# Kernel optimization log

Hardware: AMD Instinct MI355X
Metric: run time of the kernel (lower is better)

## Reference

```python
import jax, jax.numpy as jnp
from jax import lax
import numpy as np

S = 2048      # seq_len
E = 1024      # embedding_dim
H = 512       # hidden per direction (hidden_dim // 2)
V = 50000     # vocab
T = 16        # tagset_size
START, STOP = 0, 1
NEG = -10000.0


def setup_inputs() -> dict:
    key = jax.random.key(0)
    ks = jax.random.split(key, 20)
    bound = 1.0 / np.sqrt(H)

    def u(k, shape):
        return jax.random.uniform(k, shape, minval=-bound, maxval=bound, dtype=jnp.float32)

    sentence = jax.random.randint(ks[0], (S,), 0, V)
    emb = jax.random.normal(ks[1], (V, E), dtype=jnp.float32) * 0.1
    # PyTorch LSTM weights, gate order (i, f, g, o) stacked along first dim
    Wih_f = u(ks[2], (4 * H, E)); Whh_f = u(ks[3], (4 * H, H))
    bih_f = u(ks[4], (4 * H,));   bhh_f = u(ks[5], (4 * H,))
    Wih_b = u(ks[6], (4 * H, E)); Whh_b = u(ks[7], (4 * H, H))
    bih_b = u(ks[8], (4 * H,));   bhh_b = u(ks[9], (4 * H,))
    # init_hidden(): randn initial (h0, c0), [2 directions, H] (batch=1 squeezed)
    h0 = jax.random.normal(ks[10], (2, H), dtype=jnp.float32)
    c0 = jax.random.normal(ks[11], (2, H), dtype=jnp.float32)
    Wout = u(ks[12], (T, 2 * H)); bout = u(ks[13], (T,))
    transitions = jax.random.normal(ks[14], (T, T), dtype=jnp.float32)
    transitions = transitions.at[START, :].set(NEG).at[:, STOP].set(NEG)
    return dict(sentence=sentence, emb=emb,
                Wih_f=Wih_f, Whh_f=Whh_f, bih_f=bih_f, bhh_f=bhh_f,
                Wih_b=Wih_b, Whh_b=Whh_b, bih_b=bih_b, bhh_b=bhh_b,
                h0=h0, c0=c0, Wout=Wout, bout=bout, transitions=transitions)


def _lstm_dir(x, Wih, Whh, bih, bhh, h0, c0):
    # x: [S, E] -> hs: [S, H]; PyTorch gate order i, f, g, o
    xg = x @ Wih.T + bih + bhh  # precompute input contribution [S, 4H]

    def step(carry, xg_t):
        h, c = carry
        g = xg_t + h @ Whh.T
        i, f, gg, o = jnp.split(g, 4)
        i, f, o = jax.nn.sigmoid(i), jax.nn.sigmoid(f), jax.nn.sigmoid(o)
        c = f * c + i * jnp.tanh(gg)
        h = o * jnp.tanh(c)
        return (h, c), h

    _, hs = lax.scan(step, (h0, c0), xg)
    return hs


def _feats(sentence, emb, Wih_f, Whh_f, bih_f, bhh_f, Wih_b, Whh_b, bih_b, bhh_b,
           h0, c0, Wout, bout):
    x = emb[sentence]  # [S, E]
    hf = _lstm_dir(x, Wih_f, Whh_f, bih_f, bhh_f, h0[0], c0[0])              # [S, H]
    hb = _lstm_dir(x[::-1], Wih_b, Whh_b, bih_b, bhh_b, h0[1], c0[1])[::-1]  # [S, H]
    out = jnp.concatenate([hf, hb], axis=-1)  # [S, 2H]
    return out @ Wout.T + bout                # [S, T]


def _viterbi(feats, transitions):
    v0 = jnp.full((T,), NEG, dtype=feats.dtype).at[START].set(0.0)

    def vstep(v, feat):
        scores = v[None, :] + transitions        # [T(next), T(prev)]
        bp = jnp.argmax(scores, axis=1)          # best prev tag per next tag
        v_new = jnp.max(scores, axis=1) + feat
        return v_new, bp

    v, bps = lax.scan(vstep, v0, feats)          # bps: [S, T]
    terminal = v + transitions[STOP]
    best = jnp.argmax(terminal)
    path_score = terminal[best]

    def btstep(tag, bp):
        return bp[tag], tag

    _, path = lax.scan(btstep, best, bps, reverse=True)  # path[t] = tag at t
    return path_score, path


def reference(sentence, emb, Wih_f, Whh_f, bih_f, bhh_f, Wih_b, Whh_b, bih_b, bhh_b,
              h0, c0, Wout, bout, transitions):
    feats = _feats(sentence, emb, Wih_f, Whh_f, bih_f, bhh_f,
                   Wih_b, Whh_b, bih_b, bhh_b, h0, c0, Wout, bout)
    path_score, path = _viterbi(feats, transitions)
    return path_score, path
```

## Files before the change

kernel.cpp:

```cpp
#include <hip/hip_runtime.h>
#include <hip/hip_bf16.h>

#define S 2048
#define NEGV -10000.0f

typedef unsigned long long ull;
typedef unsigned int uint4v __attribute__((ext_vector_type(4)));

__device__ __forceinline__ float fsig(float x) {
  return 1.0f / (1.0f + __expf(-x));
}
__device__ __forceinline__ float ftanh(float x) {
  float a = fabsf(x);
  float e = __expf(-2.0f * a);
  float r = (1.0f - e) / (1.0f + e);
  return copysignf(r, x);
}

__global__ void init_k(const float* __restrict__ h0, ull* __restrict__ hbuf,
                       int* __restrict__ flags) {
  int b = blockIdx.x, u = threadIdx.x;
  if (b < 2) {
    ull pk = (1ULL << 32) | (ull)__float_as_uint(h0[b * 512 + u]);
    __hip_atomic_store(&hbuf[b * 1024 + u], pk, __ATOMIC_RELAXED, __HIP_MEMORY_SCOPE_AGENT);
    __hip_atomic_store(&hbuf[b * 1024 + 512 + u], 0ULL, __ATOMIC_RELAXED, __HIP_MEMORY_SCOPE_AGENT);
  } else {
    __hip_atomic_store(&flags[(b - 2) * 512 + u], 0, __ATOMIC_RELAXED, __HIP_MEMORY_SCOPE_AGENT);
    if (b == 2 && u < 2)
      __hip_atomic_store(&flags[2048 + u], 0, __ATOMIC_RELAXED, __HIP_MEMORY_SCOPE_AGENT);
  }
}

__device__ __forceinline__ ull compose_map(ull a, ull b) {
  ull r = 0;
  #pragma unroll
  for (int i = 0; i < 16; ++i) {
    int bi = (int)((b >> (4 * i)) & 15);
    int ai = (int)((a >> (4 * bi)) & 15);
    r |= (ull)ai << (4 * i);
  }
  return r;
}

__global__ __launch_bounds__(256) void fused_k(
    const int* __restrict__ sent, const float* __restrict__ emb,
    const float* __restrict__ Wih_f, const float* __restrict__ Wih_b,
    const float* __restrict__ bih_f, const float* __restrict__ bhh_f,
    const float* __restrict__ bih_b, const float* __restrict__ bhh_b,
    const float* __restrict__ Whh_f, const float* __restrict__ Whh_b,
    const float* __restrict__ c0,
    const float* __restrict__ Wout, const float* __restrict__ bout,
    const float* __restrict__ trans,
    float* __restrict__ xg,
    ull* __restrict__ hbuf,
    float* __restrict__ hs_cat,
    float* __restrict__ feats,
    int* __restrict__ flags,
    float* __restrict__ out)
{
  __shared__ __align__(16) float smem[9232];
  const int t = threadIdx.x;

  if (blockIdx.x >= 128) {
    float* Asm = smem;
    float* Bsm = smem + 2304;
    int*   sidx = (int*)(smem + 4480);
    const int tm = t >> 4, tn = t & 15;
    const int lr = t >> 2, lkq = t & 3;

    for (int i = 0; i < 16; ++i) {
      const int T = (blockIdx.x - 128) + 128 * i;
      const int byo = T >> 6, bxo = T & 63;
      const int by = (byo & 1) ? (31 - (byo >> 1)) : (byo >> 1);
      const int bx = (bxo & 1) ? (32 + (bxo >> 1)) : (bxo >> 1);
      const int n0 = bx * 64, m0 = by * 64;

      const float* W = (n0 < 2048) ? (Wih_f + (size_t)n0 * 1024)
                                   : (Wih_b + (size_t)(n0 - 2048) * 1024);
      __syncthreads();
      if (t < 64) sidx[t] = sent[m0 + t];
      __syncthreads();

      float acc[4][4] = {};
      for (int k0 = 0; k0 < 1024; k0 += 32) {
        const float* ap = emb + (size_t)sidx[lr] * 1024 + k0 + lkq * 8;
        float4 a0 = *(const float4*)ap;
        float4 a1 = *(const float4*)(ap + 4);
        const float* bp = W + (size_t)lr * 1024 + k0 + lkq * 8;
        float4 b0 = *(const float4*)bp;
        float4 b1 = *(const float4*)(bp + 4);
        __syncthreads();
        *(float4*)&Asm[lr * 36 + lkq * 8]     = a0;
        *(float4*)&Asm[lr * 36 + lkq * 8 + 4] = a1;
        {
          const float* bb0 = (const float*)&b0;
          const float* bb1 = (const float*)&b1;
          #pragma unroll
          for (int j = 0; j < 4; ++j) Bsm[(lkq * 8 + j) * 68 + lr] = bb0[j];
          #pragma unroll
          for (int j = 0; j < 4; ++j) Bsm[(lkq * 8 + 4 + j) * 68 + lr] = bb1[j];
        }
        __syncthreads();
        #pragma unroll
        for (int kk = 0; kk < 32; ++kk) {
          float a0_ = Asm[(tm * 4 + 0) * 36 + kk];
          float a1_ = Asm[(tm * 4 + 1) * 36 + kk];
          float a2_ = Asm[(tm * 4 + 2) * 36 + kk];
          float a3_ = Asm[(tm * 4 + 3) * 36 + kk];
          float4 bv = *(const float4*)&Bsm[kk * 68 + tn * 4];
          acc[0][0] = fmaf(a0_, bv.x, acc[0][0]); acc[0][1] = fmaf(a0_, bv.y, acc[0][1]);
          acc[0][2] = fmaf(a0_, bv.z, acc[0][2]); acc[0][3] = fmaf(a0_, bv.w, acc[0][3]);
          acc[1][0] = fmaf(a1_, bv.x, acc[1][0]); acc[1][1] = fmaf(a1_, bv.y, acc[1][1]);
          acc[1][2] = fmaf(a1_, bv.z, acc[1][2]); acc[1][3] = fmaf(a1_, bv.w, acc[1][3]);
          acc[2][0] = fmaf(a2_, bv.x, acc[2][0]); acc[2][1] = fmaf(a2_, bv.y, acc[2][1]);
          acc[2][2] = fmaf(a2_, bv.z, acc[2][2]); acc[2][3] = fmaf(a2_, bv.w, acc[2][3]);
          acc[3][0] = fmaf(a3_, bv.x, acc[3][0]); acc[3][1] = fmaf(a3_, bv.y, acc[3][1]);
          acc[3][2] = fmaf(a3_, bv.z, acc[3][2]); acc[3][3] = fmaf(a3_, bv.w, acc[3][3]);
        }
      }

      const float* bi = (n0 < 2048) ? bih_f : bih_b;
      const float* bh = (n0 < 2048) ? bhh_f : bhh_b;
      const int nb = (n0 < 2048) ? n0 : (n0 - 2048);
      #pragma unroll
      for (int ii = 0; ii < 4; ++ii) {
        int m = m0 + tm * 4 + ii;
        #pragma unroll
        for (int j = 0; j < 4; ++j) {
          int nn = tn * 4 + j;
          float bias = bi[nb + nn] + bh[nb + nn];
          __hip_atomic_store(&xg[(size_t)m * 4096 + n0 + nn], acc[ii][j] + bias,
                             __ATOMIC_RELAXED, __HIP_MEMORY_SCOPE_AGENT);
        }
      }
      asm volatile("s_waitcnt vmcnt(0)" ::: "memory");
      __syncthreads();
      if (t == 0)
        __hip_atomic_store(&flags[by * 64 + bx], 1, __ATOMIC_RELAXED, __HIP_MEMORY_SCOPE_AGENT);
    }
    return;
  }

  {
    const int w = blockIdx.x;
    const int dir = w & 1;
    const int wid = w >> 1;
    const int rr = t >> 3;
    const int seg = t & 7;
    const int g  = rr & 3;
    const int ul = rr >> 2;
    const int unit = wid * 8 + ul;
    const int grow = g * 512 + unit;
    const int bxf  = dir * 32 + g * 8 + (wid >> 3);

    float (*h_lds)[544] = (float(*)[544])smem;

    const float* Whh = dir ? Whh_b : Whh_f;
    float wreg[64];
    {
      const float* src = Whh + (size_t)grow * 512 + seg * 64;
      #pragma unroll
      for (int j = 0; j < 16; ++j) {
        float4 v = *(const float4*)(src + j * 4);
        wreg[4 * j + 0] = v.x; wreg[4 * j + 1] = v.y;
        wreg[4 * j + 2] = v.z; wreg[4 * j + 3] = v.w;
      }
    }

    ull* hb = hbuf + dir * 1024;
    float c_reg = c0[dir * 512 + unit];

    const int u0 = t * 2;
    const int wchunk = u0 >> 6, wpos = u0 & 63;

    float xg_a = 0.0f, xg_b = 0.0f;
    if (seg == 0) {
      int by0 = dir ? 31 : 0;
      while (__hip_atomic_load(&flags[by0 * 64 + bxf], __ATOMIC_RELAXED,
                               __HIP_MEMORY_SCOPE_AGENT) != 1)
        __builtin_amdgcn_s_sleep(8);
      int r0 = dir ? (S - 1) : 0;
      int r1 = dir ? (S - 2) : 1;
      xg_a = __hip_atomic_load(&xg[(size_t)r0 * 4096 + dir * 2048 + grow],
                               __ATOMIC_RELAXED, __HIP_MEMORY_SCOPE_AGENT);
      xg_b = __hip_atomic_load(&xg[(size_t)r1 * 4096 + dir * 2048 + grow],
                               __ATOMIC_RELAXED, __HIP_MEMORY_SCOPE_AGENT);
    }

    #define LSTM_STEP(K, XG_REG)                                                  \
    {                                                                             \
      const int k = (K);                                                          \
      float xgv = XG_REG;                                                         \
      if (seg == 0 && k + 2 < S) {            \
        int rowk = dir ? (S - 3 - k) : (k + 2);                                   \
        if ((rowk & 63) == (dir ? 63 : 0)) {       \
          int byn = rowk >> 6;                                                    \
          while (__hip_atomic_load(&flags[byn * 64 + bxf], __ATOMIC_RELAXED,      \
                                   __HIP_MEMORY_SCOPE_AGENT) != 1)                \
            __builtin_amdgcn_s_sleep(8);                                          \
        }                                                                         \
        XG_REG = __hip_atomic_load(&xg[(size_t)rowk * 4096 + dir * 2048 + grow],  \
                                   __ATOMIC_RELAXED, __HIP_MEMORY_SCOPE_AGENT);   \
      }                                                                           \
           \
      {                                                                           \
        ull* src = hb + (k & 1) * 512 + u0;                                       \
        const unsigned want = (unsigned)(k + 1);                                  \
        uint4v v;                                                                 \
        asm volatile("global_load_dwordx4 %0, %1, off sc0 sc1"                    \
                     : "=v"(v) : "v"(src) : "memory");                            \
        asm volatile("s_waitcnt vmcnt(0)" ::: "memory");                          \
        while (v.y != want || v.w != want) {                                      \
          __builtin_amdgcn_s_sleep(1);                                            \
          asm volatile("global_load_dwordx4 %0, %1, off sc0 sc1"                  \
                       : "=v"(v) : "v"(src) : "memory");                          \
          asm volatile("s_waitcnt vmcnt(0)" ::: "memory");                        \
        }                                                                         \
        float* dst = &h_lds[k & 1][wchunk * 68 + wpos];                           \
        dst[0] = __uint_as_float(v.x);                                            \
        dst[1] = __uint_as_float(v.z);                                            \
      }                                                                           \
      __syncthreads();                                                            \
                                           \
      const float* hl = &h_lds[k & 1][0];                                         \
      float p0 = 0.f, p1 = 0.f, p2 = 0.f, p3 = 0.f;                               \
      const float4* h4 = (const float4*)(hl + seg * 68);                          \
      _Pragma("unroll")                                                           \
      for (int j = 0; j < 16; ++j) {                                              \
        float4 hv = h4[j];                                                        \
        p0 = fmaf(wreg[4 * j + 0], hv.x, p0);                                     \
        p1 = fmaf(wreg[4 * j + 1], hv.y, p1);                                     \
        p2 = fmaf(wreg[4 * j + 2], hv.z, p2);                                     \
        p3 = fmaf(wreg[4 * j + 3], hv.w, p3);                                     \
      }                                                                           \
      float p = (p0 + p1) + (p2 + p3) + xgv;                                      \
      p += __shfl_xor(p, 1);                                                      \
      p += __shfl_xor(p, 2);                                                      \
      p += __shfl_xor(p, 4);                                                      \
      float gb_ = __shfl_xor(p, 8);                                 \
      float gc_ = __shfl_xor(p, 16);                                \
      float gd_ = __shfl_xor(gb_, 16);                              \
      if (g == 0) {                                                               \
        float iv = fsig(p), fv = fsig(gb_), ov = fsig(gd_);                       \
        float gv = ftanh(gc_);                                                    \
        c_reg = fv * c_reg + iv * gv;                                             \
        float hv = ov * ftanh(c_reg);                                             \
        if (seg == 0) {                                                           \
          ull pk = ((ull)(unsigned)(k + 2) << 32) | (ull)__float_as_uint(hv);     \
          __hip_atomic_store(&hb[((k + 1) & 1) * 512 + unit], pk,                 \
                             __ATOMIC_RELAXED, __HIP_MEMORY_SCOPE_AGENT);         \
          int orig = dir ? (S - 1 - k) : k;                                       \
          hs_cat[(size_t)orig * 1024 + dir * 512 + unit] = hv;  \
        }                                                                         \
      }                                                                           \
    }

    for (int kk = 0; kk < S; kk += 2) {
      LSTM_STEP(kk, xg_a);
      LSTM_STEP(kk + 1, xg_b);
    }
    #undef LSTM_STEP

    asm volatile("s_waitcnt vmcnt(0)" ::: "memory");
    __syncthreads();
    {
      const int base = dir * 512 + wid * 8;
      for (int i = t; i < 16384; i += 256) {
        const int row = i >> 3, u2 = i & 7;
        float* p = &hs_cat[(size_t)row * 1024 + base + u2];
        float v = *p;
        __hip_atomic_store(p, v, __ATOMIC_RELAXED, __HIP_MEMORY_SCOPE_AGENT);
      }
    }
    asm volatile("s_waitcnt vmcnt(0)" ::: "memory");
    __syncthreads();
    if (t == 0)
      __hip_atomic_fetch_add(&flags[2048], 1, __ATOMIC_RELAXED, __HIP_MEMORY_SCOPE_AGENT);
  }

  if (t == 0) {
    while (__hip_atomic_load(&flags[2048], __ATOMIC_RELAXED,
                             __HIP_MEMORY_SCOPE_AGENT) != 128)
      __builtin_amdgcn_s_sleep(8);
  }
  __syncthreads();
  {
    const int l = t & 63;
    const int wv4 = t >> 6;
    const int j = l & 15, q = l >> 4;
    #pragma unroll
    for (int r = 0; r < 4; ++r) {
      const int tpos = blockIdx.x * 16 + wv4 * 4 + r;
      const float* h = hs_cat + (size_t)tpos * 1024 + q * 256;
      const float* wp = Wout + (size_t)j * 1024 + q * 256;
      float s = 0.f;
      #pragma unroll 8
      for (int i = 0; i < 256; i += 4) {
        float4 hv = *(const float4*)(h + i);
        float4 ww = *(const float4*)(wp + i);
        s = fmaf(hv.x, ww.x, s); s = fmaf(hv.y, ww.y, s);
        s = fmaf(hv.z, ww.z, s); s = fmaf(hv.w, ww.w, s);
      }
      s += __shfl_xor(s, 16);
      s += __shfl_xor(s, 32);
      if (q == 0)
        __hip_atomic_store(&feats[tpos * 16 + j], s + bout[j],
                           __ATOMIC_RELAXED, __HIP_MEMORY_SCOPE_AGENT);
    }
  }
  asm volatile("s_waitcnt vmcnt(0)" ::: "memory");
  __syncthreads();
  if (t == 0)
    __hip_atomic_fetch_add(&flags[2049], 1, __ATOMIC_RELAXED, __HIP_MEMORY_SCOPE_AGENT);

  if (blockIdx.x == 0) {
    if (t == 0) {
      while (__hip_atomic_load(&flags[2049], __ATOMIC_RELAXED,
                               __HIP_MEMORY_SCOPE_AGENT) != 128)
        __builtin_amdgcn_s_sleep(8);
    }
    __syncthreads();

    float* P_ls  = smem;
    float* vb    = smem + 8192;
    float* Trows = smem + 8704;
    float* vg    = smem + 8960;
    float* tslot = smem + 9216;

    if (t < 256) Trows[t] = trans[t];
    __syncthreads();

    const int G = t >> 4, r = t & 15;

    {
      float Tcol[16];
      #pragma unroll
      for (int j = 0; j < 16; ++j) Tcol[j] = Trows[j * 16 + r];

      for (int cc = 0; cc < 2; ++cc) {
        const int c = G * 2 + cc, t0 = c * 64;
        float P[16];
        {
          const float4* fr = (const float4*)&feats[t0 * 16];
          float4 fA = fr[0], fB = fr[1], fC = fr[2], fD = fr[3];
          float ff[16];
          ff[0]=fA.x; ff[1]=fA.y; ff[2]=fA.z; ff[3]=fA.w;
          ff[4]=fB.x; ff[5]=fB.y; ff[6]=fB.z; ff[7]=fB.w;
          ff[8]=fC.x; ff[9]=fC.y; ff[10]=fC.z; ff[11]=fC.w;
          ff[12]=fD.x; ff[13]=fD.y; ff[14]=fD.z; ff[15]=fD.w;
          #pragma unroll
          for (int j = 0; j < 16; ++j) P[j] = Tcol[j] + ff[j];
        }
        for (int tt = t0 + 1; tt < t0 + 64; ++tt) {
          const float4* fr = (const float4*)&feats[tt * 16];
          float4 fA = fr[0], fB = fr[1], fC = fr[2], fD = fr[3];
          float ff[16];
          ff[0]=fA.x; ff[1]=fA.y; ff[2]=fA.z; ff[3]=fA.w;
          ff[4]=fB.x; ff[5]=fB.y; ff[6]=fB.z; ff[7]=fB.w;
          ff[8]=fC.x; ff[9]=fC.y; ff[10]=fC.z; ff[11]=fC.w;
          ff[12]=fD.x; ff[13]=fD.y; ff[14]=fD.z; ff[15]=fD.w;
          float Q[16];
          #pragma unroll
          for (int j = 0; j < 16; ++j) {
            const float4 Ta = *(const float4*)&Trows[j * 16 + 0];
            const float4 Tb = *(const float4*)&Trows[j * 16 + 4];
            const float4 Tc2 = *(const float4*)&Trows[j * 16 + 8];
            const float4 Td = *(const float4*)&Trows[j * 16 + 12];
            float m0 = fmaxf(P[0]  + Ta.x,  P[1]  + Ta.y);
            float m1 = fmaxf(P[2]  + Ta.z,  P[3]  + Ta.w);
            float m2 = fmaxf(P[4]  + Tb.x,  P[5]  + Tb.y);
            float m3 = fmaxf(P[6]  + Tb.z,  P[7]  + Tb.w);
            float m4 = fmaxf(P[8]  + Tc2.x, P[9]  + Tc2.y);
            float m5 = fmaxf(P[10] + Tc2.z, P[11] + Tc2.w);
            float m6 = fmaxf(P[12] + Td.x,  P[13] + Td.y);
            float m7 = fmaxf(P[14] + Td.z,  P[15] + Td.w);
            float m = fmaxf(fmaxf(fmaxf(m0, m1), fmaxf(m2, m3)),
                            fmaxf(fmaxf(m4, m5), fmaxf(m6, m7)));
            Q[j] = m + ff[j];
          }
          #pragma unroll
          for (int j = 0; j < 16; ++j) P[j] = Q[j];
        }
        #pragma unroll
        for (int j = 0; j < 16; ++j) P_ls[c * 256 + r * 16 + j] = P[j];
      }
    }
    __syncthreads();

    if (t < 16) {
      float m = (t == 0) ? 0.0f : NEGV;
      for (int c = 0; c < 32; ++c) {
        float vv[16];
        #pragma unroll
        for (int i = 0; i < 16; ++i) vv[i] = __shfl(m, i, 16);
        float nm = vv[0] + P_ls[c * 256 + 0 * 16 + t];
        #pragma unroll
        for (int i = 1; i < 16; ++i)
          nm = fmaxf(nm, vv[i] + P_ls[c * 256 + i * 16 + t]);
        vb[c * 16 + t] = nm;
        m = nm;
      }
    }
    __syncthreads();

    {
      unsigned char* bpB = (unsigned char*)P_ls;
      float Trow[16];
      #pragma unroll
      for (int k2 = 0; k2 < 16; ++k2) Trow[k2] = Trows[r * 16 + k2];

      for (int cc = 0; cc < 2; ++cc) {
        const int c = G * 2 + cc, t0 = c * 64;
        float vcur = (c == 0) ? ((r == 0) ? 0.0f : NEGV) : vb[(c - 1) * 16 + r];
        float fnext = feats[t0 * 16 + r];
        for (int tt = t0; tt < t0 + 64; ++tt) {
          float f = fnext;
          if (tt + 1 < t0 + 64) fnext = feats[(tt + 1) * 16 + r];
          float vv[16];
          #pragma unroll
          for (int i = 0; i < 16; ++i) vv[i] = __shfl(vcur, i, 16);
          float m = vv[0] + Trow[0]; int mi = 0;
          #pragma unroll
          for (int i = 1; i < 16; ++i) {
            float s2 = vv[i] + Trow[i];
            if (s2 > m) { m = s2; mi = i; }
          }
          vcur = m + f;
          bpB[tt * 16 + r] = (unsigned char)mi;
        }
      }
    }
    __syncthreads();

    if (t < 16) {
      float term = vb[31 * 16 + t] + trans[16 + t];
      int ti = t;
      #pragma unroll
      for (int mask = 1; mask <= 8; mask <<= 1) {
        float om = __shfl_xor(term, mask);
        int omi = __shfl_xor(ti, mask);
        if (om > term || (om == term && omi < ti)) { term = om; ti = omi; }
      }
      if (t == 0) { tslot[0] = term; tslot[1] = __int_as_float(ti); }
    }
    __syncthreads();

    if (t < 64) {
      const unsigned char* bpB = (const unsigned char*)P_ls;
      const int l = t;
      ull M = 0;
      {
        const int tb = 32 * l + 31;
        #pragma unroll
        for (int j = 0; j < 16; ++j)
          M |= (ull)(bpB[tb * 16 + j] & 15) << (4 * j);
      }
      for (int i = 30; i >= 0; --i) {
        const int ta = 32 * l + i;
        ull Mn = 0;
        #pragma unroll
        for (int j = 0; j < 16; ++j) {
          int idx = (int)((M >> (4 * j)) & 15);
          Mn |= (ull)(bpB[ta * 16 + idx] & 15) << (4 * j);
        }
        M = Mn;
      }
      ull Sm = M;
      #pragma unroll
      for (int d = 1; d < 64; d <<= 1) {
        ull o = __shfl_down(Sm, d);
        if (l + d < 64) Sm = compose_map(Sm, o);
      }
      ull Gm = __shfl_down(Sm, 1);
      if (l == 63) Gm = 0xFEDCBA9876543210ULL;

      int ti = __float_as_int(tslot[1]);
      int cur = (int)((Gm >> (4 * ti)) & 15);
      for (int i = 31; i >= 1; --i) {
        int tt2 = 32 * l + i;
        out[1 + tt2] = (float)cur;
        cur = bpB[tt2 * 16 + cur] & 15;
      }
      out[1 + 32 * l] = (float)cur;
      if (l == 0) out[0] = tslot[0];
    }
  }
}

extern "C" void kernel_launch(void* const* d_in, const int* in_sizes, int n_in,
                              void* d_out, int out_size, void* d_ws, size_t ws_size,
                              hipStream_t stream) {
  const int*   sent  = (const int*)d_in[0];
  const float* emb   = (const float*)d_in[1];
  const float* Wih_f = (const float*)d_in[2];
  const float* Whh_f = (const float*)d_in[3];
  const float* bih_f = (const float*)d_in[4];
  const float* bhh_f = (const float*)d_in[5];
  const float* Wih_b = (const float*)d_in[6];
  const float* Whh_b = (const float*)d_in[7];
  const float* bih_b = (const float*)d_in[8];
  const float* bhh_b = (const float*)d_in[9];
  const float* h0    = (const float*)d_in[10];
  const float* c0    = (const float*)d_in[11];
  const float* Wout  = (const float*)d_in[12];
  const float* bout  = (const float*)d_in[13];
  const float* trans = (const float*)d_in[14];
  float* out = (float*)d_out;

  char* ws = (char*)d_ws;
  float* xg     = (float*)(ws);
  float* hs_cat = (float*)(ws + 33554432);
  float* feats  = (float*)(ws + 41943040);
  ull*   hbuf   = (ull*)  (ws + 42074112);
  int*   flags  = (int*)  (ws + 42090496);

  init_k<<<6, 512, 0, stream>>>(h0, hbuf, flags);
  fused_k<<<256, 256, 0, stream>>>(sent, emb, Wih_f, Wih_b, bih_f, bhh_f,
                                   bih_b, bhh_b, Whh_f, Whh_b, c0, Wout, bout,
                                   trans, xg, hbuf, hs_cat, feats, flags, out);
}
```

Measured before the change: 3.474 ms.

## Overlap output projection with LSTM recurrence via per-chunk completion flags

The LSTM blocks now publish each 64-step chunk of hidden states as they are produced and bump a per-chunk counter. The idle xg-GEMM blocks then compute feats for each chunk as soon as both directions have finished it, so the output projection no longer runs after the whole recurrence. Chunks are handled in the order both directions complete them, starting from the middle. This adds a sync and store pass every 64 steps in the latency-critical recurrence loop, which may lengthen the serial path.

```diff
diff --git a/kernel.cpp b/kernel.cpp
--- a/kernel.cpp
+++ b/kernel.cpp
@@ -26,8 +26,6 @@
     __hip_atomic_store(&hbuf[b * 1024 + 512 + u], 0ULL, __ATOMIC_RELAXED, __HIP_MEMORY_SCOPE_AGENT);
   } else {
     __hip_atomic_store(&flags[(b - 2) * 512 + u], 0, __ATOMIC_RELAXED, __HIP_MEMORY_SCOPE_AGENT);
-    if (b == 2 && u < 2)
-      __hip_atomic_store(&flags[2048 + u], 0, __ATOMIC_RELAXED, __HIP_MEMORY_SCOPE_AGENT);
   }
 }
 
@@ -62,81 +60,122 @@
   const int t = threadIdx.x;
 
   if (blockIdx.x >= 128) {
-    float* Asm = smem;
-    float* Bsm = smem + 2304;
-    int*   sidx = (int*)(smem + 4480);
-    const int tm = t >> 4, tn = t & 15;
-    const int lr = t >> 2, lkq = t & 3;
-
-    for (int i = 0; i < 16; ++i) {
-      const int T = (blockIdx.x - 128) + 128 * i;
-      const int byo = T >> 6, bxo = T & 63;
-      const int by = (byo & 1) ? (31 - (byo >> 1)) : (byo >> 1);
-      const int bx = (bxo & 1) ? (32 + (bxo >> 1)) : (bxo >> 1);
-      const int n0 = bx * 64, m0 = by * 64;
-
-      const float* W = (n0 < 2048) ? (Wih_f + (size_t)n0 * 1024)
-                                   : (Wih_b + (size_t)(n0 - 2048) * 1024);
+    {
+      float* Asm = smem;
+      float* Bsm = smem + 2304;
+      int*   sidx = (int*)(smem + 4480);
+      const int tm = t >> 4, tn = t & 15;
+      const int lr = t >> 2, lkq = t & 3;
+
+      for (int i = 0; i < 16; ++i) {
+        const int T = (blockIdx.x - 128) + 128 * i;
+        const int byo = T >> 6, bxo = T & 63;
+        const int by = (byo & 1) ? (31 - (byo >> 1)) : (byo >> 1);
+        const int bx = (bxo & 1) ? (32 + (bxo >> 1)) : (bxo >> 1);
+        const int n0 = bx * 64, m0 = by * 64;
+
+        const float* W = (n0 < 2048) ? (Wih_f + (size_t)n0 * 1024)
+                                     : (Wih_b + (size_t)(n0 - 2048) * 1024);
+        __syncthreads();
+        if (t < 64) sidx[t] = sent[m0 + t];
+        __syncthreads();
+
+        float acc[4][4] = {};
+        for (int k0 = 0; k0 < 1024; k0 += 32) {
+          const float* ap = emb + (size_t)sidx[lr] * 1024 + k0 + lkq * 8;
+          float4 a0 = *(const float4*)ap;
+          float4 a1 = *(const float4*)(ap + 4);
+          const float* bp = W + (size_t)lr * 1024 + k0 + lkq * 8;
+          float4 b0 = *(const float4*)bp;
+          float4 b1 = *(const float4*)(bp + 4);
+          __syncthreads();
+          *(float4*)&Asm[lr * 36 + lkq * 8]     = a0;
+          *(float4*)&Asm[lr * 36 + lkq * 8 + 4] = a1;
+          {
+            const float* bb0 = (const float*)&b0;
+            const float* bb1 = (const float*)&b1;
+            #pragma unroll
+            for (int j = 0; j < 4; ++j) Bsm[(lkq * 8 + j) * 68 + lr] = bb0[j];
+            #pragma unroll
+            for (int j = 0; j < 4; ++j) Bsm[(lkq * 8 + 4 + j) * 68 + lr] = bb1[j];
+          }
+          __syncthreads();
+          #pragma unroll
+          for (int kk = 0; kk < 32; ++kk) {
+            float a0_ = Asm[(tm * 4 + 0) * 36 + kk];
+            float a1_ = Asm[(tm * 4 + 1) * 36 + kk];
+            float a2_ = Asm[(tm * 4 + 2) * 36 + kk];
+            float a3_ = Asm[(tm * 4 + 3) * 36 + kk];
+            float4 bv = *(const float4*)&Bsm[kk * 68 + tn * 4];
+            acc[0][0] = fmaf(a0_, bv.x, acc[0][0]); acc[0][1] = fmaf(a0_, bv.y, acc[0][1]);
+            acc[0][2] = fmaf(a0_, bv.z, acc[0][2]); acc[0][3] = fmaf(a0_, bv.w, acc[0][3]);
+            acc[1][0] = fmaf(a1_, bv.x, acc[1][0]); acc[1][1] = fmaf(a1_, bv.y, acc[1][1]);
+            acc[1][2] = fmaf(a1_, bv.z, acc[1][2]); acc[1][3] = fmaf(a1_, bv.w, acc[1][3]);
+            acc[2][0] = fmaf(a2_, bv.x, acc[2][0]); acc[2][1] = fmaf(a2_, bv.y, acc[2][1]);
+            acc[2][2] = fmaf(a2_, bv.z, acc[2][2]); acc[2][3] = fmaf(a2_, bv.w, acc[2][3]);
+            acc[3][0] = fmaf(a3_, bv.x, acc[3][0]); acc[3][1] = fmaf(a3_, bv.y, acc[3][1]);
+            acc[3][2] = fmaf(a3_, bv.z, acc[3][2]); acc[3][3] = fmaf(a3_, bv.w, acc[3][3]);
+          }
+        }
+
+        const float* bi = (n0 < 2048) ? bih_f : bih_b;
+        const float* bh = (n0 < 2048) ? bhh_f : bhh_b;
+        const int nb = (n0 < 2048) ? n0 : (n0 - 2048);
+        #pragma unroll
+        for (int ii = 0; ii < 4; ++ii) {
+          int m = m0 + tm * 4 + ii;
+          #pragma unroll
+          for (int j = 0; j < 4; ++j) {
+            int nn = tn * 4 + j;
+            float bias = bi[nb + nn] + bh[nb + nn];
+            __hip_atomic_store(&xg[(size_t)m * 4096 + n0 + nn], acc[ii][j] + bias,
+                               __ATOMIC_RELAXED, __HIP_MEMORY_SCOPE_AGENT);
+          }
+        }
+        asm volatile("s_waitcnt vmcnt(0)" ::: "memory");
+        __syncthreads();
+        if (t == 0)
+          __hip_atomic_store(&flags[by * 64 + bx], 1, __ATOMIC_RELAXED, __HIP_MEMORY_SCOPE_AGENT);
+      }
+    }
+
+    {
+      const int gb = blockIdx.x - 128;
+      const int rank = gb >> 2, sub = gb & 3;
+      const int c = (rank & 1) ? (16 + (rank >> 1)) : (15 - (rank >> 1));
+
+      if (t == 0) {
+        while (__hip_atomic_load(&flags[2064 + c * 16], __ATOMIC_RELAXED,
+                                 __HIP_MEMORY_SCOPE_AGENT) != 128)
+          __builtin_amdgcn_s_sleep(32);
+      }
       __syncthreads();
-      if (t < 64) sidx[t] = sent[m0 + t];
-      __syncthreads();
-
-      float acc[4][4] = {};
-      for (int k0 = 0; k0 < 1024; k0 += 32) {
-        const float* ap = emb + (size_t)sidx[lr] * 1024 + k0 + lkq * 8;
-        float4 a0 = *(const float4*)ap;
-        float4 a1 = *(const float4*)(ap + 4);
-        const float* bp = W + (size_t)lr * 1024 + k0 + lkq * 8;
-        float4 b0 = *(const float4*)bp;
-        float4 b1 = *(const float4*)(bp + 4);
-        __syncthreads();
-        *(float4*)&Asm[lr * 36 + lkq * 8]     = a0;
-        *(float4*)&Asm[lr * 36 + lkq * 8 + 4] = a1;
-        {
-          const float* bb0 = (const float*)&b0;
-          const float* bb1 = (const float*)&b1;
-          #pragma unroll
-          for (int j = 0; j < 4; ++j) Bsm[(lkq * 8 + j) * 68 + lr] = bb0[j];
-          #pragma unroll
-          for (int j = 0; j < 4; ++j) Bsm[(lkq * 8 + 4 + j) * 68 + lr] = bb1[j];
-        }
-        __syncthreads();
-        #pragma unroll
-        for (int kk = 0; kk < 32; ++kk) {
-          float a0_ = Asm[(tm * 4 + 0) * 36 + kk];
-          float a1_ = Asm[(tm * 4 + 1) * 36 + kk];
-          float a2_ = Asm[(tm * 4 + 2) * 36 + kk];
-          float a3_ = Asm[(tm * 4 + 3) * 36 + kk];
-          float4 bv = *(const float4*)&Bsm[kk * 68 + tn * 4];
-          acc[0][0] = fmaf(a0_, bv.x, acc[0][0]); acc[0][1] = fmaf(a0_, bv.y, acc[0][1]);
-          acc[0][2] = fmaf(a0_, bv.z, acc[0][2]); acc[0][3] = fmaf(a0_, bv.w, acc[0][3]);
-          acc[1][0] = fmaf(a1_, bv.x, acc[1][0]); acc[1][1] = fmaf(a1_, bv.y, acc[1][1]);
-          acc[1][2] = fmaf(a1_, bv.z, acc[1][2]); acc[1][3] = fmaf(a1_, bv.w, acc[1][3]);
-          acc[2][0] = fmaf(a2_, bv.x, acc[2][0]); acc[2][1] = fmaf(a2_, bv.y, acc[2][1]);
-          acc[2][2] = fmaf(a2_, bv.z, acc[2][2]); acc[2][3] = fmaf(a2_, bv.w, acc[2][3]);
-          acc[3][0] = fmaf(a3_, bv.x, acc[3][0]); acc[3][1] = fmaf(a3_, bv.y, acc[3][1]);
-          acc[3][2] = fmaf(a3_, bv.z, acc[3][2]); acc[3][3] = fmaf(a3_, bv.w, acc[3][3]);
-        }
-      }
-
-      const float* bi = (n0 < 2048) ? bih_f : bih_b;
-      const float* bh = (n0 < 2048) ? bhh_f : bhh_b;
-      const int nb = (n0 < 2048) ? n0 : (n0 - 2048);
+
+      const int l = t & 63;
+      const int wv4 = t >> 6;
+      const int j = l & 15, q = l >> 4;
       #pragma unroll
-      for (int ii = 0; ii < 4; ++ii) {
-        int m = m0 + tm * 4 + ii;
-        #pragma unroll
-        for (int j = 0; j < 4; ++j) {
-          int nn = tn * 4 + j;
-          float bias = bi[nb + nn] + bh[nb + nn];
-          __hip_atomic_store(&xg[(size_t)m * 4096 + n0 + nn], acc[ii][j] + bias,
+      for (int r = 0; r < 4; ++r) {
+        const int tpos = c * 64 + sub * 16 + wv4 * 4 + r;
+        const float* h = hs_cat + (size_t)tpos * 1024 + q * 256;
+        const float* wp = Wout + (size_t)j * 1024 + q * 256;
+        float s = 0.f;
+        #pragma unroll 8
+        for (int i = 0; i < 256; i += 4) {
+          float4 hv = *(const float4*)(h + i);
+          float4 ww = *(const float4*)(wp + i);
+          s = fmaf(hv.x, ww.x, s); s = fmaf(hv.y, ww.y, s);
+          s = fmaf(hv.z, ww.z, s); s = fmaf(hv.w, ww.w, s);
+        }
+        s += __shfl_xor(s, 16);
+        s += __shfl_xor(s, 32);
+        if (q == 0)
+          __hip_atomic_store(&feats[tpos * 16 + j], s + bout[j],
                              __ATOMIC_RELAXED, __HIP_MEMORY_SCOPE_AGENT);
-        }
-      }
-      asm volatile("s_waitcnt vmcnt(0)" ::: "memory");
+      }
       __syncthreads();
       if (t == 0)
-        __hip_atomic_store(&flags[by * 64 + bx], 1, __ATOMIC_RELAXED, __HIP_MEMORY_SCOPE_AGENT);
+        __hip_atomic_fetch_add(&flags[2049], 1, __ATOMIC_RELAXED, __HIP_MEMORY_SCOPE_AGENT);
     }
     return;
   }
@@ -258,62 +297,31 @@
     for (int kk = 0; kk < S; kk += 2) {
       LSTM_STEP(kk, xg_a);
       LSTM_STEP(kk + 1, xg_b);
+
+      if ((kk & 63) == 62) {
+        const int c = dir ? ((S - 2 - kk) >> 6) : ((kk + 1) >> 6);
+        __syncthreads();
+        {
+          const int base2 = dir * 512 + wid * 8;
+          const int i2 = t * 2;
+          const int rl = i2 >> 3, u2 = i2 & 7;
+          float* p = &hs_cat[(size_t)(c * 64 + rl) * 1024 + base2 + u2];
+          float v0 = p[0], v1 = p[1];
+          __hip_atomic_store(p,     v0, __ATOMIC_RELAXED, __HIP_MEMORY_SCOPE_AGENT);
+          __hip_atomic_store(p + 1, v1, __ATOMIC_RELAXED, __HIP_MEMORY_SCOPE_AGENT);
+        }
+        __syncthreads();
+        if (t == 0)
+          __hip_atomic_fetch_add(&flags[2064 + c * 16], 1,
+                                 __ATOMIC_RELAXED, __HIP_MEMORY_SCOPE_AGENT);
+      }
     }
     #undef LSTM_STEP
-
-    asm volatile("s_waitcnt vmcnt(0)" ::: "memory");
-    __syncthreads();
-    {
-      const int base = dir * 512 + wid * 8;
-      for (int i = t; i < 16384; i += 256) {
-        const int row = i >> 3, u2 = i & 7;
-        float* p = &hs_cat[(size_t)row * 1024 + base + u2];
-        float v = *p;
-        __hip_atomic_store(p, v, __ATOMIC_RELAXED, __HIP_MEMORY_SCOPE_AGENT);
-      }
-    }
-    asm volatile("s_waitcnt vmcnt(0)" ::: "memory");
-    __syncthreads();
-    if (t == 0)
-      __hip_atomic_fetch_add(&flags[2048], 1, __ATOMIC_RELAXED, __HIP_MEMORY_SCOPE_AGENT);
   }
 
-  if (t == 0) {
-    while (__hip_atomic_load(&flags[2048], __ATOMIC_RELAXED,
-                             __HIP_MEMORY_SCOPE_AGENT) != 128)
-      __builtin_amdgcn_s_sleep(8);
-  }
-  __syncthreads();
+  if (blockIdx.x != 0) return;
+
   {
-    const int l = t & 63;
-    const int wv4 = t >> 6;
-    const int j = l & 15, q = l >> 4;
-    #pragma unroll
-    for (int r = 0; r < 4; ++r) {
-      const int tpos = blockIdx.x * 16 + wv4 * 4 + r;
-      const float* h = hs_cat + (size_t)tpos * 1024 + q * 256;
-      const float* wp = Wout + (size_t)j * 1024 + q * 256;
-      float s = 0.f;
-      #pragma unroll 8
-      for (int i = 0; i < 256; i += 4) {
-        float4 hv = *(const float4*)(h + i);
-        float4 ww = *(const float4*)(wp + i);
-        s = fmaf(hv.x, ww.x, s); s = fmaf(hv.y, ww.y, s);
-        s = fmaf(hv.z, ww.z, s); s = fmaf(hv.w, ww.w, s);
-      }
-      s += __shfl_xor(s, 16);
-      s += __shfl_xor(s, 32);
-      if (q == 0)
-        __hip_atomic_store(&feats[tpos * 16 + j], s + bout[j],
-                           __ATOMIC_RELAXED, __HIP_MEMORY_SCOPE_AGENT);
-    }
-  }
-  asm volatile("s_waitcnt vmcnt(0)" ::: "memory");
-  __syncthreads();
-  if (t == 0)
-    __hip_atomic_fetch_add(&flags[2049], 1, __ATOMIC_RELAXED, __HIP_MEMORY_SCOPE_AGENT);
-
-  if (blockIdx.x == 0) {
     if (t == 0) {
       while (__hip_atomic_load(&flags[2049], __ATOMIC_RELAXED,
                                __HIP_MEMORY_SCOPE_AGENT) != 128)
@@ -324,7 +332,6 @@
     float* P_ls  = smem;
     float* vb    = smem + 8192;
     float* Trows = smem + 8704;
-    float* vg    = smem + 8960;
     float* tslot = smem + 9216;
 
     if (t < 256) Trows[t] = trans[t];
@@ -514,7 +521,7 @@
   ull*   hbuf   = (ull*)  (ws + 42074112);
   int*   flags  = (int*)  (ws + 42090496);
 
-  init_k<<<6, 512, 0, stream>>>(h0, hbuf, flags);
+  init_k<<<10, 512, 0, stream>>>(h0, hbuf, flags);
   fused_k<<<256, 256, 0, stream>>>(sent, emb, Wih_f, Wih_b, bih_f, bhh_f,
                                    bih_b, bhh_b, Whh_f, Whh_b, c0, Wout, bout,
                                    trans, xg, hbuf, hs_cat, feats, flags, out);
```

New measurement: 3.513 ms. No clear change (+1.1%).
